# Kernel optimization log

Measured on AMD Instinct MI355X. Metric: run time of the kernel, lower is better.

## Reference

```python
import jax, jax.numpy as jnp
import numpy as np

N = 100000
E = 1000000
IN_C = 128
HID = 128
HEADS = 4
DH = HID // HEADS
L = 2
RWSE_DIM = 16
WALK_LEN = 16
NPAIRS = 200000
EPS = 1e-5


def setup_inputs() -> dict:
    key = jax.random.key(0)
    ks = jax.random.split(key, 20)
    x = jax.random.normal(ks[0], (N, IN_C), dtype=jnp.float32)
    rw_diag = jax.random.uniform(ks[1], (N, WALK_LEN), dtype=jnp.float32)
    edge_index = jax.random.randint(ks[2], (2, E), 0, N, dtype=jnp.int32)
    src = jax.random.randint(ks[3], (NPAIRS,), 0, N, dtype=jnp.int32)
    dst = jax.random.randint(ks[4], (NPAIRS,), 0, N, dtype=jnp.int32)
    s = 0.05
    W_rwse = jax.random.normal(ks[5], (WALK_LEN, RWSE_DIM), dtype=jnp.float32) * s
    b_rwse = jnp.zeros((RWSE_DIM,), dtype=jnp.float32)
    W_in = jax.random.normal(ks[6], (IN_C + RWSE_DIM, HID), dtype=jnp.float32) * s
    b_in = jnp.zeros((HID,), dtype=jnp.float32)
    Wq = jax.random.normal(ks[7], (L, HID, HID), dtype=jnp.float32) * s
    bq = jnp.zeros((L, HID), dtype=jnp.float32)
    Wk = jax.random.normal(ks[8], (L, HID, HID), dtype=jnp.float32) * s
    bk = jnp.zeros((L, HID), dtype=jnp.float32)
    Wv = jax.random.normal(ks[9], (L, HID, HID), dtype=jnp.float32) * s
    bv = jnp.zeros((L, HID), dtype=jnp.float32)
    Ws = jax.random.normal(ks[10], (L, HID, HID), dtype=jnp.float32) * s
    bs = jnp.zeros((L, HID), dtype=jnp.float32)
    ln_g = jnp.ones((L, HID), dtype=jnp.float32)
    ln_b = jnp.zeros((L, HID), dtype=jnp.float32)
    return {"x": x, "rw_diag": rw_diag, "edge_index": edge_index, "src": src,
            "dst": dst, "W_rwse": W_rwse, "b_rwse": b_rwse, "W_in": W_in,
            "b_in": b_in, "Wq": Wq, "bq": bq, "Wk": Wk, "bk": bk, "Wv": Wv,
            "bv": bv, "Ws": Ws, "bs": bs, "ln_g": ln_g, "ln_b": ln_b}


def reference(x, rw_diag, edge_index, src, dst, W_rwse, b_rwse, W_in, b_in,
              Wq, bq, Wk, bk, Wv, bv, Ws, bs, ln_g, ln_b):
    row = edge_index[0]  # message source j
    col = edge_index[1]  # message target i
    # RWSE projection + input projection
    pe = rw_diag @ W_rwse + b_rwse                      # [N, rwse_dim]
    h = jnp.concatenate([x, pe], axis=-1) @ W_in + b_in  # [N, HID]
    scale = 1.0 / jnp.sqrt(jnp.float32(DH))
    for l in range(L):
        q = (h @ Wq[l] + bq[l]).reshape(N, HEADS, DH)
        k = (h @ Wk[l] + bk[l]).reshape(N, HEADS, DH)
        v = (h @ Wv[l] + bv[l]).reshape(N, HEADS, DH)
        # per-edge attention scores (gather)
        score = jnp.einsum('ehd,ehd->eh', q[col], k[row]) * scale  # [E, H]
        # segment softmax over incoming edges of each target node
        m = jax.ops.segment_max(score, col, num_segments=N)   # [N, H]
        ex = jnp.exp(score - m[col])
        z = jax.ops.segment_sum(ex, col, num_segments=N)      # [N, H]
        alpha = ex / z[col]                                   # [E, H]
        agg = jax.ops.segment_sum(alpha[:, :, None] * v[row], col,
                                  num_segments=N).reshape(N, HID)
        conv = agg + h @ Ws[l] + bs[l]  # root/skip linear (PyG lin_skip)
        # residual + LayerNorm + ReLU
        y = h + conv
        mu = jnp.mean(y, axis=-1, keepdims=True)
        var = jnp.mean(jnp.square(y - mu), axis=-1, keepdims=True)
        h = jax.nn.relu(ln_g[l] * (y - mu) / jnp.sqrt(var + EPS) + ln_b[l])
    logits = jnp.sum(h[src] * h[dst], axis=-1)  # [NPAIRS]
    return jax.nn.sigmoid(logits)
```

## Files before the change

### kernel.cpp

```cpp
#include <hip/hip_runtime.h>
#include <hip/hip_bf16.h>
#include <cstdint>


#define NN      100000
#define EE      1000000
#define RWSEC   16
#define WALKC   16
#define NPAIRSC 200000
#define BSH     9
#define BKT     ((NN + 511) >> BSH)

typedef unsigned int       u32;
typedef unsigned short     u16;
typedef unsigned char      u8;
typedef __attribute__((ext_vector_type(8))) short   short8;
typedef __attribute__((ext_vector_type(4))) float   f32x4;

__device__ __forceinline__ float bflo(u32 u){ return __uint_as_float(u << 16); }
__device__ __forceinline__ float bfhi(u32 u){ return __uint_as_float(u & 0xffff0000u); }
__device__ __forceinline__ u16 f2bf(float f){
    u32 u = __float_as_uint(f);
    u += 0x7fffu + ((u >> 16) & 1u);
    return (u16)(u >> 16);
}
__device__ __forceinline__ u32 pack2(float a, float b){
    return (u32)f2bf(a) | ((u32)f2bf(b) << 16);
}

#if defined(__has_builtin)
#if __has_builtin(__builtin_amdgcn_cvt_pk_f32_fp8) && __has_builtin(__builtin_amdgcn_cvt_pk_fp8_f32)
#define HWFP8 1
#endif
#if __has_builtin(__builtin_amdgcn_sdot4)
#define USE_SDOT4 1
#endif
#endif

#ifndef HWFP8
__device__ __forceinline__ float fp8dec1(u32 b){
    u32 s = (b >> 7) & 1u, e = (b >> 3) & 15u, m = b & 7u;
    float mag = e ? __uint_as_float(((e + 120u) << 23) | (m << 20))
                  : (float)m * 0.001953125f;
    return s ? -mag : mag;
}
__device__ __forceinline__ u32 fp8enc1(float f){
    u32 u = __float_as_uint(f); u32 s = (u >> 31) << 7; float a = fabsf(f);
    if (a >= 448.f) return s | 0x7Eu;
    u32 ua = __float_as_uint(a);
    ua += 0x7FFFFu + ((ua >> 20) & 1u);
    int e = (int)(ua >> 23) - 127 + 7;
    if (e <= 0){ int m = (int)rintf(a * 512.f); return s | (u32)m; }
    u32 m = (ua >> 20) & 7u;
    return s | ((u32)e << 3) | m;
}
#endif

__device__ __forceinline__ void fp8x4_dec(u32 w4, float& f0, float& f1, float& f2, float& f3){
#ifdef HWFP8
    auto lo = __builtin_amdgcn_cvt_pk_f32_fp8((int)w4, false);
    auto hi = __builtin_amdgcn_cvt_pk_f32_fp8((int)w4, true);
    f0 = lo[0]; f1 = lo[1]; f2 = hi[0]; f3 = hi[1];
#else
    f0 = fp8dec1(w4 & 255u); f1 = fp8dec1((w4 >> 8) & 255u);
    f2 = fp8dec1((w4 >> 16) & 255u); f3 = fp8dec1(w4 >> 24);
#endif
}
__device__ __forceinline__ u32 fp8x4_enc(float f0, float f1, float f2, float f3){
#ifdef HWFP8
    u32 t = (u32)__builtin_amdgcn_cvt_pk_fp8_f32(f0, f1, 0, false);
    return (u32)__builtin_amdgcn_cvt_pk_fp8_f32(f2, f3, (int)t, true);
#else
    return fp8enc1(f0) | (fp8enc1(f1) << 8) | (fp8enc1(f2) << 16) | (fp8enc1(f3) << 24);
#endif
}

#define QSCALE   48.0f
#define DESCALE  7.67259e-5f

__device__ __forceinline__ int i8q(float f){
    float c = fminf(fmaxf(f * QSCALE, -127.f), 127.f);
    return (int)rintf(c);
}
__device__ __forceinline__ u32 i8x4_enc(float f0, float f1, float f2, float f3){
    return (u32)(i8q(f0) & 255) | ((u32)(i8q(f1) & 255) << 8)
         | ((u32)(i8q(f2) & 255) << 16) | ((u32)(i8q(f3) & 255) << 24);
}

__global__ __launch_bounds__(256) void winprep_kernel(const float* __restrict__ Win,
                                                      u16* __restrict__ Winb){
    int t = blockIdx.x * 256 + threadIdx.x;
    if (t >= 8 * 5 * 64) return;
    int lane = t & 63, fi = t >> 6;
    int nt = fi / 5, kk = fi - nt * 5;
    int col = nt * 16 + (lane & 15);
    int k0  = kk * 32 + (lane >> 4) * 8;
    u16* dst = Winb + (size_t)fi * 512 + lane * 8;
    #pragma unroll
    for (int e = 0; e < 8; ++e){
        int k = k0 + e;
        dst[e] = (k < 144) ? f2bf(Win[(size_t)k * 128 + col]) : (u16)0;
    }
}

__global__ __launch_bounds__(256) void inproj_mfma(const float* __restrict__ x,
        const float* __restrict__ rw, const float* __restrict__ Wr,
        const float* __restrict__ br,
        const u16* __restrict__ Winb, const float* __restrict__ bin,
        u16* __restrict__ hb){
    __shared__ u16   hs[64 * 168];
    __shared__ float rws[64 * 16];
    __shared__ u16   ob[64 * 128];
    int tid = threadIdx.x;
    int n0  = blockIdx.x * 64;

    #pragma unroll
    for (int i = 0; i < 32; ++i){
        int g   = i * 256 + tid;
        int row = g >> 5, c4 = g & 31;
        float4 f = make_float4(0.f, 0.f, 0.f, 0.f);
        if (n0 + row < NN)
            f = *reinterpret_cast<const float4*>(x + (size_t)(n0 + row) * 128 + c4 * 4);
        *reinterpret_cast<uint2*>((char*)hs + row * 336 + c4 * 8)
            = make_uint2(pack2(f.x, f.y), pack2(f.z, f.w));
    }
    {
        int row = tid >> 2, c4 = tid & 3;
        float4 f = make_float4(0.f, 0.f, 0.f, 0.f);
        if (n0 + row < NN)
            f = *reinterpret_cast<const float4*>(rw + (size_t)(n0 + row) * 16 + c4 * 4);
        *reinterpret_cast<float4*>(&rws[row * 16 + c4 * 4]) = f;
    }
    __syncthreads();
    {
        int row = tid >> 2, j0 = (tid & 3) * 4;
        float p0 = br[j0], p1 = br[j0 + 1], p2 = br[j0 + 2], p3 = br[j0 + 3];
        #pragma unroll
        for (int w = 0; w < 16; ++w){
            float r = rws[row * 16 + w];
            const float4 wv = *reinterpret_cast<const float4*>(Wr + w * 16 + j0);
            p0 = fmaf(r, wv.x, p0); p1 = fmaf(r, wv.y, p1);
            p2 = fmaf(r, wv.z, p2); p3 = fmaf(r, wv.w, p3);
        }
        *reinterpret_cast<uint2*>((char*)hs + row * 336 + 256 + (tid & 3) * 8)
            = make_uint2(pack2(p0, p1), pack2(p2, p3));
        *reinterpret_cast<uint2*>((char*)hs + row * 336 + 288 + (tid & 3) * 8)
            = make_uint2(0u, 0u);
    }
    __syncthreads();

    int l = tid & 63, w = tid >> 6;
    int r16 = l & 15, kq = l >> 4;
    short8 ha[4][5];
    #pragma unroll
    for (int rg = 0; rg < 4; ++rg)
        #pragma unroll
        for (int kk = 0; kk < 5; ++kk){
            int row = rg * 16 + r16;
            ha[rg][kk] = *reinterpret_cast<const short8*>(
                (const char*)hs + row * 336 + kk * 64 + kq * 16);
        }
    #pragma unroll
    for (int nt2 = 0; nt2 < 2; ++nt2){
        int nt = w * 2 + nt2;
        const short8* wfrag = reinterpret_cast<const short8*>(Winb) + (size_t)(nt * 5) * 64;
        f32x4 acc[4];
        #pragma unroll
        for (int rg = 0; rg < 4; ++rg) acc[rg] = (f32x4){0.f, 0.f, 0.f, 0.f};
        #pragma unroll
        for (int kk = 0; kk < 5; ++kk){
            short8 wf = wfrag[kk * 64 + l];
            #pragma unroll
            for (int rg = 0; rg < 4; ++rg)
                acc[rg] = __builtin_amdgcn_mfma_f32_16x16x32_bf16(wf, ha[rg][kk], acc[rg], 0, 0, 0);
        }
        float4 bvv = *reinterpret_cast<const float4*>(bin + nt * 16 + kq * 4);
        #pragma unroll
        for (int rg = 0; rg < 4; ++rg){
            u32 p0 = pack2(acc[rg][0] + bvv.x, acc[rg][1] + bvv.y);
            u32 p1 = pack2(acc[rg][2] + bvv.z, acc[rg][3] + bvv.w);
            int row = rg * 16 + r16;
            int cb  = (nt * 32 + kq * 8) ^ ((row & 7) << 4);
            *reinterpret_cast<uint2*>((char*)ob + row * 256 + cb) = make_uint2(p0, p1);
        }
    }
    __syncthreads();
    #pragma unroll
    for (int i = 0; i < 4; ++i){
        int row = i * 16 + (tid >> 4);
        int cb  = (tid & 15) * 16;
        uint4 v = *reinterpret_cast<const uint4*>(
            (char*)ob + row * 256 + (cb ^ ((row & 7) << 4)));
        if (n0 + row < NN)
            *reinterpret_cast<uint4*>(hb + (size_t)(n0 + row) * 128 + cb / 2) = v;
    }
}

__global__ __launch_bounds__(256) void bhist_kernel(const int* __restrict__ col,
                                                    int* __restrict__ bcnt){
    __shared__ int h[BKT];
    int tid = threadIdx.x;
    for (int i = tid; i < BKT; i += 256) h[i] = 0;
    __syncthreads();
    for (int e = blockIdx.x * 256 + tid; e < EE; e += gridDim.x * 256)
        atomicAdd(&h[col[e] >> BSH], 1);
    __syncthreads();
    for (int i = tid; i < BKT; i += 256)
        if (h[i]) atomicAdd(&bcnt[i], h[i]);
}

__global__ __launch_bounds__(256) void bscan_kernel(const int* __restrict__ bcnt,
                                                    int* __restrict__ bstart,
                                                    int* __restrict__ bwork){
    __shared__ int lds[256];
    int tid = threadIdx.x;
    int v = (tid < BKT) ? bcnt[tid] : 0;
    lds[tid] = v;
    __syncthreads();
    for (int off = 1; off < 256; off <<= 1){
        int y = (tid >= off) ? lds[tid - off] : 0;
        __syncthreads();
        lds[tid] += y;
        __syncthreads();
    }
    if (tid < BKT){ int p = lds[tid] - v; bstart[tid] = p; bwork[tid] = p; }
}

__global__ __launch_bounds__(256) void bpart_kernel(const int* __restrict__ ei,
                                                    int* __restrict__ bwork,
                                                    u32* __restrict__ bkt){
    __shared__ int cnt_[BKT], base_[BKT], rnk_[BKT];
    int tid = threadIdx.x;
    for (int i = tid; i < BKT; i += 256){ cnt_[i] = 0; rnk_[i] = 0; }
    __syncthreads();
    for (int e = blockIdx.x * 256 + tid; e < EE; e += gridDim.x * 256)
        atomicAdd(&cnt_[ei[EE + e] >> BSH], 1);
    __syncthreads();
    for (int i = tid; i < BKT; i += 256)
        base_[i] = cnt_[i] ? atomicAdd(&bwork[i], cnt_[i]) : 0;
    __syncthreads();
    for (int e = blockIdx.x * 256 + tid; e < EE; e += gridDim.x * 256){
        int c = ei[EE + e], b = c >> BSH;
        int p = base_[b] + atomicAdd(&rnk_[b], 1);
        bkt[p] = ((u32)ei[e] << BSH) | (u32)(c & 511);
    }
}

__global__ __launch_bounds__(256) void bcsr_kernel(const int* __restrict__ bstart,
                                                   const int* __restrict__ bcnt,
                                                   const u32* __restrict__ bkt,
                                                   int* __restrict__ offs,
                                                   int* __restrict__ deg,
                                                   int* __restrict__ ebuf){
    __shared__ int dcnt[512];
    __shared__ int pref[512];
    __shared__ int psum[256];
    int b   = blockIdx.x;
    int tid = threadIdx.x;
    int n0  = b << BSH;
    int nb  = NN - n0 < 512 ? NN - n0 : 512;
    int e0  = bstart[b];
    int ec  = bcnt[b];
    dcnt[tid] = 0; dcnt[tid + 256] = 0;
    __syncthreads();
    for (int i = tid; i < ec; i += 256)
        atomicAdd(&dcnt[bkt[e0 + i] & 511u], 1);
    __syncthreads();
    int s0 = dcnt[2 * tid], s1 = dcnt[2 * tid + 1];
    psum[tid] = s0 + s1;
    __syncthreads();
    for (int off = 1; off < 256; off <<= 1){
        int y = (tid >= off) ? psum[tid - off] : 0;
        __syncthreads();
        psum[tid] += y;
        __syncthreads();
    }
    int exq = psum[tid] - (s0 + s1);
    pref[2 * tid]     = exq;
    pref[2 * tid + 1] = exq + s0;
    __syncthreads();
    for (int i = tid; i < nb; i += 256){
        offs[n0 + i] = e0 + pref[i];
        deg[n0 + i]  = dcnt[i];
    }
    __syncthreads();
    for (int i = tid; i < ec; i += 256){
        u32 rc = bkt[e0 + i];
        int p = atomicAdd(&pref[rc & 511u], 1);
        ebuf[e0 + p] = (int)(rc >> BSH);
    }
}

__global__ __launch_bounds__(256) void wprep_kernel(const float* __restrict__ Wq,
        const float* __restrict__ Wk, const float* __restrict__ Wv,
        const float* __restrict__ Ws, u16* __restrict__ Wb2){
    int t = blockIdx.x * 256 + threadIdx.x;
    if (t >= 2 * 128 * 64) return;
    int lane = t & 63, fi = (t >> 6) & 127, l = t >> 13;
    int gnt = fi >> 2, kk = fi & 3;
    int m = gnt >> 3;
    int col = (gnt * 16 + (lane & 15)) & 127;
    const float* W = (m == 0 ? Wq : m == 1 ? Wk : m == 2 ? Wv : Ws) + (size_t)l * 16384;
    int k0 = kk * 32 + (lane >> 4) * 8;
    u16* dst = Wb2 + ((size_t)l * 128 + fi) * 512 + lane * 8;
    #pragma unroll
    for (int e = 0; e < 8; ++e) dst[e] = f2bf(W[(size_t)(k0 + e) * 128 + col]);
}

__global__ __launch_bounds__(256) void gemm4_mfma(const u16* __restrict__ hb,
        const u16* __restrict__ Wb2,
        const float* __restrict__ bq, const float* __restrict__ bk,
        const float* __restrict__ bv, const float* __restrict__ bs,
        u16* __restrict__ qb, u8* __restrict__ kvb, u16* __restrict__ hsb){
    __shared__ u16 hs[64 * 128];
    __shared__ u16 ob[4][64 * 128];
    int tid = threadIdx.x;
    int n0  = blockIdx.x * 64;
    #pragma unroll
    for (int i = 0; i < 4; ++i){
        int c = i * 256 + tid;
        int row = c >> 4, cb = (c & 15) * 16;
        uint4 v = make_uint4(0u, 0u, 0u, 0u);
        if (n0 + row < NN)
            v = *reinterpret_cast<const uint4*>(hb + (size_t)(n0 + row) * 128 + cb / 2);
        *reinterpret_cast<uint4*>((char*)hs + row * 256 + (cb ^ ((row & 7) << 4))) = v;
    }
    __syncthreads();
    int l = tid & 63, w = tid >> 6;
    int r16 = l & 15, kq = l >> 4;
    short8 ha[4][4];
    #pragma unroll
    for (int rg = 0; rg < 4; ++rg)
        #pragma unroll
        for (int kk = 0; kk < 4; ++kk){
            int row = rg * 16 + r16;
            int byt = (kk * 64 + kq * 16) ^ ((row & 7) << 4);
            ha[rg][kk] = *reinterpret_cast<const short8*>((const char*)hs + row * 256 + byt);
        }
    const float* bp = w == 0 ? bq : w == 1 ? bk : w == 2 ? bv : bs;
    const short8* wfrag = reinterpret_cast<const short8*>(Wb2) + (size_t)(w * 8) * 4 * 64;
    u16* myob = &ob[w][0];
    #pragma unroll
    for (int nt = 0; nt < 8; ++nt){
        f32x4 acc[4];
        #pragma unroll
        for (int rg = 0; rg < 4; ++rg) acc[rg] = (f32x4){0.f, 0.f, 0.f, 0.f};
        #pragma unroll
        for (int kk = 0; kk < 4; ++kk){
            short8 wf = wfrag[(nt * 4 + kk) * 64 + l];
            #pragma unroll
            for (int rg = 0; rg < 4; ++rg)
                acc[rg] = __builtin_amdgcn_mfma_f32_16x16x32_bf16(wf, ha[rg][kk], acc[rg], 0, 0, 0);
        }
        float4 bvv = *reinterpret_cast<const float4*>(bp + nt * 16 + kq * 4);
        #pragma unroll
        for (int rg = 0; rg < 4; ++rg){
            int row = rg * 16 + r16;
            int cb  = (nt * 32 + kq * 8) ^ ((row & 7) << 4);
            float a0 = acc[rg][0] + bvv.x, a1 = acc[rg][1] + bvv.y;
            float a2 = acc[rg][2] + bvv.z, a3 = acc[rg][3] + bvv.w;
            if (w == 3){
                uint2 hval = *reinterpret_cast<const uint2*>((const char*)hs + row * 256 + cb);
                a0 += bflo(hval.x); a1 += bfhi(hval.x);
                a2 += bflo(hval.y); a3 += bfhi(hval.y);
            }
            *reinterpret_cast<uint2*>((char*)myob + row * 256 + cb)
                = make_uint2(pack2(a0, a1), pack2(a2, a3));
        }
    }
    asm volatile("s_waitcnt lgkmcnt(0)" ::: "memory");
    if (w == 1 || w == 2){
        int off = (w == 2) ? 8 : 0;
        #pragma unroll
        for (int i = 0; i < 16; ++i){
            int row = i * 4 + kq;
            int cb  = r16 * 16;
            uint4 v = *reinterpret_cast<const uint4*>(
                (char*)myob + row * 256 + (cb ^ ((row & 7) << 4)));
            if (n0 + row < NN){
                u32 A, B;
#ifdef USE_SDOT4
                if (w == 1){
                    A = i8x4_enc(bflo(v.x), bfhi(v.x), bflo(v.y), bfhi(v.y));
                    B = i8x4_enc(bflo(v.z), bfhi(v.z), bflo(v.w), bfhi(v.w));
                } else
#endif
                {
                    A = fp8x4_enc(bflo(v.x), bfhi(v.x), bflo(v.y), bfhi(v.y));
                    B = fp8x4_enc(bflo(v.z), bfhi(v.z), bflo(v.w), bfhi(v.w));
                }
                *reinterpret_cast<uint2*>((char*)kvb + (size_t)(n0 + row) * 256
                                          + r16 * 16 + off) = make_uint2(A, B);
            }
        }
    } else {
        u16* outp = (w == 0) ? qb : hsb;
        #pragma unroll
        for (int i = 0; i < 16; ++i){
            int row = i * 4 + kq;
            int cb  = r16 * 16;
            uint4 v = *reinterpret_cast<const uint4*>(
                (char*)myob + row * 256 + (cb ^ ((row & 7) << 4)));
            if (n0 + row < NN)
                *reinterpret_cast<uint4*>(outp + (size_t)(n0 + row) * 128 + cb / 2) = v;
        }
    }
}

__global__ __launch_bounds__(256) void attn_kernel(u16* __restrict__ hb,
        const u16* __restrict__ qb, const u8* __restrict__ kvb,
        const u16* __restrict__ hsb,
        const int* __restrict__ offs, const int* __restrict__ deg,
        const int* __restrict__ ebuf,
        const float* __restrict__ gw, const float* __restrict__ bta){
    int tid  = threadIdx.x;
    int lane = tid & 63;
    int n    = blockIdx.x * 4 + (tid >> 6);
    int eq = lane >> 4, gq = lane & 15;
    uint4 qu = *reinterpret_cast<const uint4*>(qb + (size_t)n * 128 + gq * 8);
#ifdef USE_SDOT4
    int qi0 = (int)i8x4_enc(bflo(qu.x), bfhi(qu.x), bflo(qu.y), bfhi(qu.y));
    int qi1 = (int)i8x4_enc(bflo(qu.z), bfhi(qu.z), bflo(qu.w), bfhi(qu.w));
#else
    const float scale = 0.17677669529663687f;
    float q0 = bflo(qu.x) * scale, q1 = bfhi(qu.x) * scale;
    float q2 = bflo(qu.y) * scale, q3 = bfhi(qu.y) * scale;
    float q4 = bflo(qu.z) * scale, q5 = bfhi(qu.z) * scale;
    float q6 = bflo(qu.w) * scale, q7 = bfhi(qu.w) * scale;
#endif
    int beg = offs[n], cnt = deg[n];
    float z = 0.f;
    float a0 = 0.f, a1 = 0.f, a2 = 0.f, a3 = 0.f;
    float a4 = 0.f, a5 = 0.f, a6 = 0.f, a7 = 0.f;

#ifdef USE_SDOT4
    #define SCORE(kv)                                                                 \
        float s;                                                                      \
        {   int si = __builtin_amdgcn_sdot4((int)kv.x, qi0, 0, false);                \
            si = __builtin_amdgcn_sdot4((int)kv.y, qi1, si, false);                   \
            s = (float)si * DESCALE; }
#else
    #define SCORE(kv)                                                                 \
        float s;                                                                      \
        {   float k0,k1,k2,k3,k4,k5,k6,k7;                                            \
            fp8x4_dec(kv.x, k0, k1, k2, k3); fp8x4_dec(kv.y, k4, k5, k6, k7);         \
            s = q0*k0 + q1*k1 + q2*k2 + q3*k3 + q4*k4 + q5*k5 + q6*k6 + q7*k7; }
#endif

    #define EDGE4(r_)                                                                 \
    {   uint4 kv = *reinterpret_cast<const uint4*>(kvb + (size_t)(r_) * 256 + gq * 16); \
        SCORE(kv);                                                                    \
        s += __shfl_xor(s, 1); s += __shfl_xor(s, 2);                                 \
        float ex = __expf(s);                                                         \
        float v0,v1,v2,v3,v4,v5,v6,v7;                                                \
        fp8x4_dec(kv.z, v0, v1, v2, v3); fp8x4_dec(kv.w, v4, v5, v6, v7);             \
        z += ex;                                                                      \
        a0 = fmaf(ex, v0, a0); a1 = fmaf(ex, v1, a1);                                 \
        a2 = fmaf(ex, v2, a2); a3 = fmaf(ex, v3, a3);                                 \
        a4 = fmaf(ex, v4, a4); a5 = fmaf(ex, v5, a5);                                 \
        a6 = fmaf(ex, v6, a6); a7 = fmaf(ex, v7, a7);  }

    int t = 0;
    for (; t + 8 <= cnt; t += 8){
        int ra = ebuf[beg + t + eq];
        int rb = ebuf[beg + t + 4 + eq];
        EDGE4(ra);
        EDGE4(rb);
    }
    if (t + 4 <= cnt){
        int ra = ebuf[beg + t + eq];
        EDGE4(ra);
        t += 4;
    }
    if (t < cnt){
        int idx = t + eq;
        int r = ebuf[beg + (idx < cnt ? idx : cnt - 1)];
        uint4 kv = *reinterpret_cast<const uint4*>(kvb + (size_t)r * 256 + gq * 16);
        SCORE(kv);
        s += __shfl_xor(s, 1); s += __shfl_xor(s, 2);
        float ex = (idx < cnt) ? __expf(s) : 0.f;
        float v0,v1,v2,v3,v4,v5,v6,v7;
        fp8x4_dec(kv.z, v0, v1, v2, v3); fp8x4_dec(kv.w, v4, v5, v6, v7);
        z += ex;
        a0 = fmaf(ex, v0, a0); a1 = fmaf(ex, v1, a1);
        a2 = fmaf(ex, v2, a2); a3 = fmaf(ex, v3, a3);
        a4 = fmaf(ex, v4, a4); a5 = fmaf(ex, v5, a5);
        a6 = fmaf(ex, v6, a6); a7 = fmaf(ex, v7, a7);
    }
    #undef EDGE4
    #undef SCORE

    z  += __shfl_xor(z, 16);  z  += __shfl_xor(z, 32);
    a0 += __shfl_xor(a0, 16); a0 += __shfl_xor(a0, 32);
    a1 += __shfl_xor(a1, 16); a1 += __shfl_xor(a1, 32);
    a2 += __shfl_xor(a2, 16); a2 += __shfl_xor(a2, 32);
    a3 += __shfl_xor(a3, 16); a3 += __shfl_xor(a3, 32);
    a4 += __shfl_xor(a4, 16); a4 += __shfl_xor(a4, 32);
    a5 += __shfl_xor(a5, 16); a5 += __shfl_xor(a5, 32);
    a6 += __shfl_xor(a6, 16); a6 += __shfl_xor(a6, 32);
    a7 += __shfl_xor(a7, 16); a7 += __shfl_xor(a7, 32);
    float rz = (cnt > 0) ? 1.f / z : 0.f;

    size_t p = (size_t)n * 128 + gq * 8;
    uint4 hu = *reinterpret_cast<const uint4*>(hsb + p);
    float y0 = bflo(hu.x) + a0 * rz, y1 = bfhi(hu.x) + a1 * rz;
    float y2 = bflo(hu.y) + a2 * rz, y3 = bfhi(hu.y) + a3 * rz;
    float y4 = bflo(hu.z) + a4 * rz, y5 = bfhi(hu.z) + a5 * rz;
    float y6 = bflo(hu.w) + a6 * rz, y7 = bfhi(hu.w) + a7 * rz;
    float sum = y0 + y1 + y2 + y3 + y4 + y5 + y6 + y7;
    float sq  = y0*y0 + y1*y1 + y2*y2 + y3*y3 + y4*y4 + y5*y5 + y6*y6 + y7*y7;
    #pragma unroll
    for (int m = 1; m < 16; m <<= 1){
        sum += __shfl_xor(sum, m);
        sq  += __shfl_xor(sq,  m);
    }
    float mu  = sum * (1.f / 128.f);
    float var = sq * (1.f / 128.f) - mu * mu;
    var = var < 0.f ? 0.f : var;
    float inv = rsqrtf(var + 1e-5f);
    int c = gq * 8;
    float4 gm0 = *reinterpret_cast<const float4*>(gw + c);
    float4 gm1 = *reinterpret_cast<const float4*>(gw + c + 4);
    float4 bt0 = *reinterpret_cast<const float4*>(bta + c);
    float4 bt1 = *reinterpret_cast<const float4*>(bta + c + 4);
    float o0 = fmaf(gm0.x * (y0 - mu), inv, bt0.x);
    float o1 = fmaf(gm0.y * (y1 - mu), inv, bt0.y);
    float o2 = fmaf(gm0.z * (y2 - mu), inv, bt0.z);
    float o3 = fmaf(gm0.w * (y3 - mu), inv, bt0.w);
    float o4 = fmaf(gm1.x * (y4 - mu), inv, bt1.x);
    float o5 = fmaf(gm1.y * (y5 - mu), inv, bt1.y);
    float o6 = fmaf(gm1.z * (y6 - mu), inv, bt1.z);
    float o7 = fmaf(gm1.w * (y7 - mu), inv, bt1.w);
    o0 = o0 > 0.f ? o0 : 0.f;  o1 = o1 > 0.f ? o1 : 0.f;
    o2 = o2 > 0.f ? o2 : 0.f;  o3 = o3 > 0.f ? o3 : 0.f;
    o4 = o4 > 0.f ? o4 : 0.f;  o5 = o5 > 0.f ? o5 : 0.f;
    o6 = o6 > 0.f ? o6 : 0.f;  o7 = o7 > 0.f ? o7 : 0.f;
    if (eq == 0)
        *reinterpret_cast<uint4*>(hb + p) = make_uint4(
            pack2(o0, o1), pack2(o2, o3), pack2(o4, o5), pack2(o6, o7));
}

__global__ __launch_bounds__(256) void pair_kernel(const u16* __restrict__ hb,
                                                   const int* __restrict__ src,
                                                   const int* __restrict__ dst,
                                                   float* __restrict__ out){
    int tid = threadIdx.x;
    int pid = blockIdx.x * 16 + (tid >> 4);
    int sub = tid & 15;
    int s = src[pid], d = dst[pid];
    uint4 a = *reinterpret_cast<const uint4*>(hb + (size_t)s * 128 + sub * 8);
    uint4 b = *reinterpret_cast<const uint4*>(hb + (size_t)d * 128 + sub * 8);
    float dot = bflo(a.x) * bflo(b.x) + bfhi(a.x) * bfhi(b.x)
              + bflo(a.y) * bflo(b.y) + bfhi(a.y) * bfhi(b.y)
              + bflo(a.z) * bflo(b.z) + bfhi(a.z) * bfhi(b.z)
              + bflo(a.w) * bflo(b.w) + bfhi(a.w) * bfhi(b.w);
    dot += __shfl_xor(dot, 1); dot += __shfl_xor(dot, 2);
    dot += __shfl_xor(dot, 4); dot += __shfl_xor(dot, 8);
    if (sub == 0) out[pid] = 1.f / (1.f + __expf(-dot));
}

extern "C" void kernel_launch(void* const* d_in, const int* in_sizes, int n_in,
                              void* d_out, int out_size, void* d_ws, size_t ws_size,
                              hipStream_t stream){
    const float* x      = (const float*)d_in[0];
    const float* rw     = (const float*)d_in[1];
    const int*   ei     = (const int*)  d_in[2];
    const int*   src    = (const int*)  d_in[3];
    const int*   dst    = (const int*)  d_in[4];
    const float* W_rwse = (const float*)d_in[5];
    const float* b_rwse = (const float*)d_in[6];
    const float* W_in   = (const float*)d_in[7];
    const float* b_in   = (const float*)d_in[8];
    const float* Wq     = (const float*)d_in[9];
    const float* bq     = (const float*)d_in[10];
    const float* Wk     = (const float*)d_in[11];
    const float* bk     = (const float*)d_in[12];
    const float* Wv     = (const float*)d_in[13];
    const float* bv     = (const float*)d_in[14];
    const float* Wsk    = (const float*)d_in[15];
    const float* bsk    = (const float*)d_in[16];
    const float* ln_g   = (const float*)d_in[17];
    const float* ln_b   = (const float*)d_in[18];
    float* out = (float*)d_out;

    char* p = (char*)d_ws;
    auto carve = [&](size_t bytes) -> char* {
        char* r = p; p += (bytes + 255) & ~(size_t)255; return r;
    };
    u16*   hb    = (u16*) carve((size_t)NN * 128 * 2);
    u16*   qb    = (u16*) carve((size_t)NN * 128 * 2);
    u8*    kvb   = (u8*)  carve((size_t)NN * 256);
    u16*   hsb   = (u16*) carve((size_t)NN * 128 * 2);
    int*   offs  = (int*) carve((size_t)NN * 4);
    int*   deg   = (int*) carve((size_t)NN * 4);
    int*   ebuf  = (int*) carve((size_t)EE * 4);
    u32*   bkt   = (u32*) carve((size_t)EE * 4);
    int*   bcnt  = (int*) carve((size_t)BKT * 4);
    int*   bstart= (int*) carve((size_t)BKT * 4);
    int*   bwork = (int*) carve((size_t)BKT * 4);
    u16*   Wb2   = (u16*) carve((size_t)2 * 128 * 512 * 2);
    u16*   Winb  = (u16*) carve((size_t)8 * 5 * 512 * 2);

    hipMemsetAsync(bcnt, 0, (size_t)BKT * 4, stream);

    winprep_kernel<<<10, 256, 0, stream>>>(W_in, Winb);
    wprep_kernel<<<64, 256, 0, stream>>>(Wq, Wk, Wv, Wsk, Wb2);
    inproj_mfma<<<(NN + 63) / 64, 256, 0, stream>>>(x, rw, W_rwse, b_rwse,
                                                    Winb, b_in, hb);
    bhist_kernel<<<512, 256, 0, stream>>>(ei + EE, bcnt);
    bscan_kernel<<<1, 256, 0, stream>>>(bcnt, bstart, bwork);
    bpart_kernel<<<512, 256, 0, stream>>>(ei, bwork, bkt);
    bcsr_kernel<<<BKT, 256, 0, stream>>>(bstart, bcnt, bkt, offs, deg, ebuf);

    for (int l = 0; l < 2; ++l){
        gemm4_mfma<<<(NN + 63) / 64, 256, 0, stream>>>(hb, Wb2 + (size_t)l * 65536,
            bq + l * 128, bk + l * 128, bv + l * 128, bsk + l * 128,
            qb, kvb, hsb);
        attn_kernel<<<NN / 4, 256, 0, stream>>>(hb, qb, kvb, hsb,
            offs, deg, ebuf, ln_g + l * 128, ln_b + l * 128);
    }
    pair_kernel<<<NPAIRSC / 16, 256, 0, stream>>>(hb, src, dst, out);
}
```

Measured before the change: 340.9 us.

## Store Q as int8, accumulate attention values in packed fp16

The GEMM kernel now quantizes Q to int8 at write time, so the attention kernel reads 8 bytes per lane instead of 16 and skips re-quantizing. The attention accumulation switches from eight fp32 FMAs per edge to four packed fp16 FMAs, with fp8 values converted straight to half pairs. Softmax uses exp2 with the log2(e) factor folded into the descale constant, and the tail edge path reuses the same macro. The fp16 accumulators and unnormalized exp weights risk precision loss or overflow on high-degree nodes.

After: 334.2 us. About the same (-2.0%).

```diff
diff --git a/kernel.cpp b/kernel.cpp
--- a/kernel.cpp
+++ b/kernel.cpp
@@ -14,8 +14,9 @@
 typedef unsigned int       u32;
 typedef unsigned short     u16;
 typedef unsigned char      u8;
-typedef __attribute__((ext_vector_type(8))) short   short8;
-typedef __attribute__((ext_vector_type(4))) float   f32x4;
+typedef __attribute__((ext_vector_type(8))) short    short8;
+typedef __attribute__((ext_vector_type(4))) float    f32x4;
+typedef __attribute__((ext_vector_type(2))) _Float16 h2;
 
 __device__ __forceinline__ float bflo(u32 u){ return __uint_as_float(u << 16); }
 __device__ __forceinline__ float bfhi(u32 u){ return __uint_as_float(u & 0xffff0000u); }
@@ -34,6 +35,9 @@
 #endif
 #if __has_builtin(__builtin_amdgcn_sdot4)
 #define USE_SDOT4 1
+#endif
+#if __has_builtin(__builtin_amdgcn_cvt_pk_f16_fp8)
+#define HWF16FP8 1
 #endif
 #endif
 
@@ -74,9 +78,25 @@
     return fp8enc1(f0) | (fp8enc1(f1) << 8) | (fp8enc1(f2) << 16) | (fp8enc1(f3) << 24);
 #endif
 }
-
-#define QSCALE   48.0f
-#define DESCALE  7.67259e-5f
+__device__ __forceinline__ void fp8x4_to_h2(u32 w, h2& lo, h2& hi){
+#ifdef HWF16FP8
+    lo = __builtin_bit_cast(h2, __builtin_amdgcn_cvt_pk_f16_fp8((int)w, false));
+    hi = __builtin_bit_cast(h2, __builtin_amdgcn_cvt_pk_f16_fp8((int)w, true));
+#else
+    float f0, f1, f2, f3;
+    fp8x4_dec(w, f0, f1, f2, f3);
+    lo = __builtin_bit_cast(h2, __builtin_amdgcn_cvt_pkrtz(f0, f1));
+    hi = __builtin_bit_cast(h2, __builtin_amdgcn_cvt_pkrtz(f2, f3));
+#endif
+}
+__device__ __forceinline__ h2 h2shfl_add(h2 a, int m){
+    int u = __builtin_bit_cast(int, a);
+    int o = __shfl_xor(u, m);
+    return a + __builtin_bit_cast(h2, o);
+}
+
+#define QSCALE    48.0f
+#define DESCALE2  1.10693e-4f
 
 __device__ __forceinline__ int i8q(float f){
     float c = fminf(fmaxf(f * QSCALE, -127.f), 127.f);
@@ -85,6 +105,9 @@
 __device__ __forceinline__ u32 i8x4_enc(float f0, float f1, float f2, float f3){
     return (u32)(i8q(f0) & 255) | ((u32)(i8q(f1) & 255) << 8)
          | ((u32)(i8q(f2) & 255) << 16) | ((u32)(i8q(f3) & 255) << 24);
+}
+__device__ __forceinline__ float sb(u32 w, int i){
+    return (float)(int)(signed char)((w >> (i * 8)) & 255u);
 }
 
 __global__ __launch_bounds__(256) void winprep_kernel(const float* __restrict__ Win,
@@ -311,7 +334,7 @@
         const u16* __restrict__ Wb2,
         const float* __restrict__ bq, const float* __restrict__ bk,
         const float* __restrict__ bv, const float* __restrict__ bs,
-        u16* __restrict__ qb, u8* __restrict__ kvb, u16* __restrict__ hsb){
+        u8* __restrict__ qb, u8* __restrict__ kvb, u16* __restrict__ hsb){
     __shared__ u16 hs[64 * 128];
     __shared__ u16 ob[4][64 * 128];
     int tid = threadIdx.x;
@@ -393,8 +416,25 @@
                                           + r16 * 16 + off) = make_uint2(A, B);
             }
         }
+    } else if (w == 0){
+        #pragma unroll
+        for (int i = 0; i < 16; ++i){
+            int row = i * 4 + kq;
+            int cb  = r16 * 16;
+            uint4 v = *reinterpret_cast<const uint4*>(
+                (char*)myob + row * 256 + (cb ^ ((row & 7) << 4)));
+            if (n0 + row < NN){
+#ifdef USE_SDOT4
+                u32 A = i8x4_enc(bflo(v.x), bfhi(v.x), bflo(v.y), bfhi(v.y));
+                u32 B = i8x4_enc(bflo(v.z), bfhi(v.z), bflo(v.w), bfhi(v.w));
+                *reinterpret_cast<uint2*>(qb + (size_t)(n0 + row) * 128 + cb / 2)
+                    = make_uint2(A, B);
+#else
+                *reinterpret_cast<uint4*>((u16*)qb + (size_t)(n0 + row) * 128 + cb / 2) = v;
+#endif
+            }
+        }
     } else {
-        u16* outp = (w == 0) ? qb : hsb;
         #pragma unroll
         for (int i = 0; i < 16; ++i){
             int row = i * 4 + kq;
@@ -402,13 +442,13 @@
             uint4 v = *reinterpret_cast<const uint4*>(
                 (char*)myob + row * 256 + (cb ^ ((row & 7) << 4)));
             if (n0 + row < NN)
-                *reinterpret_cast<uint4*>(outp + (size_t)(n0 + row) * 128 + cb / 2) = v;
+                *reinterpret_cast<uint4*>(hsb + (size_t)(n0 + row) * 128 + cb / 2) = v;
         }
     }
 }
 
 __global__ __launch_bounds__(256) void attn_kernel(u16* __restrict__ hb,
-        const u16* __restrict__ qb, const u8* __restrict__ kvb,
+        const u8* __restrict__ qb, const u8* __restrict__ kvb,
         const u16* __restrict__ hsb,
         const int* __restrict__ offs, const int* __restrict__ deg,
         const int* __restrict__ ebuf,
@@ -417,12 +457,12 @@
     int lane = tid & 63;
     int n    = blockIdx.x * 4 + (tid >> 6);
     int eq = lane >> 4, gq = lane & 15;
-    uint4 qu = *reinterpret_cast<const uint4*>(qb + (size_t)n * 128 + gq * 8);
 #ifdef USE_SDOT4
-    int qi0 = (int)i8x4_enc(bflo(qu.x), bfhi(qu.x), bflo(qu.y), bfhi(qu.y));
-    int qi1 = (int)i8x4_enc(bflo(qu.z), bfhi(qu.z), bflo(qu.w), bfhi(qu.w));
+    uint2 qu = *reinterpret_cast<const uint2*>(qb + (size_t)n * 128 + gq * 8);
+    int qi0 = (int)qu.x, qi1 = (int)qu.y;
 #else
     const float scale = 0.17677669529663687f;
+    uint4 qu = *reinterpret_cast<const uint4*>((const u16*)qb + (size_t)n * 128 + gq * 8);
     float q0 = bflo(qu.x) * scale, q1 = bfhi(qu.x) * scale;
     float q2 = bflo(qu.y) * scale, q3 = bfhi(qu.y) * scale;
     float q4 = bflo(qu.z) * scale, q5 = bfhi(qu.z) * scale;
@@ -430,76 +470,68 @@
 #endif
     int beg = offs[n], cnt = deg[n];
     float z = 0.f;
-    float a0 = 0.f, a1 = 0.f, a2 = 0.f, a3 = 0.f;
-    float a4 = 0.f, a5 = 0.f, a6 = 0.f, a7 = 0.f;
+    h2 acc01 = (h2)0, acc23 = (h2)0, acc45 = (h2)0, acc67 = (h2)0;
 
 #ifdef USE_SDOT4
     #define SCORE(kv)                                                                 \
         float s;                                                                      \
         {   int si = __builtin_amdgcn_sdot4((int)kv.x, qi0, 0, false);                \
             si = __builtin_amdgcn_sdot4((int)kv.y, qi1, si, false);                   \
-            s = (float)si * DESCALE; }
+            s = (float)si * DESCALE2; }
 #else
     #define SCORE(kv)                                                                 \
         float s;                                                                      \
-        {   float k0,k1,k2,k3,k4,k5,k6,k7;                                            \
-            fp8x4_dec(kv.x, k0, k1, k2, k3); fp8x4_dec(kv.y, k4, k5, k6, k7);         \
-            s = q0*k0 + q1*k1 + q2*k2 + q3*k3 + q4*k4 + q5*k5 + q6*k6 + q7*k7; }
-#endif
-
-    #define EDGE4(r_)                                                                 \
+        {   s = q0*sb(kv.x,0) + q1*sb(kv.x,1) + q2*sb(kv.x,2) + q3*sb(kv.x,3)         \
+              + q4*sb(kv.y,0) + q5*sb(kv.y,1) + q6*sb(kv.y,2) + q7*sb(kv.y,3);        \
+            s *= (1.4426950408889634f / QSCALE); }
+#endif
+
+    #define EDGE4(r_, ok_)                                                            \
     {   uint4 kv = *reinterpret_cast<const uint4*>(kvb + (size_t)(r_) * 256 + gq * 16); \
         SCORE(kv);                                                                    \
         s += __shfl_xor(s, 1); s += __shfl_xor(s, 2);                                 \
-        float ex = __expf(s);                                                         \
-        float v0,v1,v2,v3,v4,v5,v6,v7;                                                \
-        fp8x4_dec(kv.z, v0, v1, v2, v3); fp8x4_dec(kv.w, v4, v5, v6, v7);             \
+        float ex = (ok_) ? exp2f(s) : 0.f;                                            \
+        h2 v01, v23, v45, v67;                                                        \
+        fp8x4_to_h2(kv.z, v01, v23);                                                  \
+        fp8x4_to_h2(kv.w, v45, v67);                                                  \
         z += ex;                                                                      \
-        a0 = fmaf(ex, v0, a0); a1 = fmaf(ex, v1, a1);                                 \
-        a2 = fmaf(ex, v2, a2); a3 = fmaf(ex, v3, a3);                                 \
-        a4 = fmaf(ex, v4, a4); a5 = fmaf(ex, v5, a5);                                 \
-        a6 = fmaf(ex, v6, a6); a7 = fmaf(ex, v7, a7);  }
+        _Float16 exh = (_Float16)ex;                                                  \
+        h2 exv = {exh, exh};                                                          \
+        acc01 = __builtin_elementwise_fma(exv, v01, acc01);                           \
+        acc23 = __builtin_elementwise_fma(exv, v23, acc23);                           \
+        acc45 = __builtin_elementwise_fma(exv, v45, acc45);                           \
+        acc67 = __builtin_elementwise_fma(exv, v67, acc67);  }
 
     int t = 0;
     for (; t + 8 <= cnt; t += 8){
         int ra = ebuf[beg + t + eq];
         int rb = ebuf[beg + t + 4 + eq];
-        EDGE4(ra);
-        EDGE4(rb);
+        EDGE4(ra, true);
+        EDGE4(rb, true);
     }
     if (t + 4 <= cnt){
         int ra = ebuf[beg + t + eq];
-        EDGE4(ra);
+        EDGE4(ra, true);
         t += 4;
     }
     if (t < cnt){
         int idx = t + eq;
         int r = ebuf[beg + (idx < cnt ? idx : cnt - 1)];
-        uint4 kv = *reinterpret_cast<const uint4*>(kvb + (size_t)r * 256 + gq * 16);
-        SCORE(kv);
-        s += __shfl_xor(s, 1); s += __shfl_xor(s, 2);
-        float ex = (idx < cnt) ? __expf(s) : 0.f;
-        float v0,v1,v2,v3,v4,v5,v6,v7;
-        fp8x4_dec(kv.z, v0, v1, v2, v3); fp8x4_dec(kv.w, v4, v5, v6, v7);
-        z += ex;
-        a0 = fmaf(ex, v0, a0); a1 = fmaf(ex, v1, a1);
-        a2 = fmaf(ex, v2, a2); a3 = fmaf(ex, v3, a3);
-        a4 = fmaf(ex, v4, a4); a5 = fmaf(ex, v5, a5);
-        a6 = fmaf(ex, v6, a6); a7 = fmaf(ex, v7, a7);
+        EDGE4(r, idx < cnt);
     }
     #undef EDGE4
     #undef SCORE
 
-    z  += __shfl_xor(z, 16);  z  += __shfl_xor(z, 32);
-    a0 += __shfl_xor(a0, 16); a0 += __shfl_xor(a0, 32);
-    a1 += __shfl_xor(a1, 16); a1 += __shfl_xor(a1, 32);
-    a2 += __shfl_xor(a2, 16); a2 += __shfl_xor(a2, 32);
-    a3 += __shfl_xor(a3, 16); a3 += __shfl_xor(a3, 32);
-    a4 += __shfl_xor(a4, 16); a4 += __shfl_xor(a4, 32);
-    a5 += __shfl_xor(a5, 16); a5 += __shfl_xor(a5, 32);
-    a6 += __shfl_xor(a6, 16); a6 += __shfl_xor(a6, 32);
-    a7 += __shfl_xor(a7, 16); a7 += __shfl_xor(a7, 32);
+    z += __shfl_xor(z, 16);  z += __shfl_xor(z, 32);
+    acc01 = h2shfl_add(acc01, 16); acc01 = h2shfl_add(acc01, 32);
+    acc23 = h2shfl_add(acc23, 16); acc23 = h2shfl_add(acc23, 32);
+    acc45 = h2shfl_add(acc45, 16); acc45 = h2shfl_add(acc45, 32);
+    acc67 = h2shfl_add(acc67, 16); acc67 = h2shfl_add(acc67, 32);
     float rz = (cnt > 0) ? 1.f / z : 0.f;
+    float a0 = (float)acc01[0], a1 = (float)acc01[1];
+    float a2 = (float)acc23[0], a3 = (float)acc23[1];
+    float a4 = (float)acc45[0], a5 = (float)acc45[1];
+    float a6 = (float)acc67[0], a7 = (float)acc67[1];
 
     size_t p = (size_t)n * 128 + gq * 8;
     uint4 hu = *reinterpret_cast<const uint4*>(hsb + p);
@@ -588,7 +620,7 @@
         char* r = p; p += (bytes + 255) & ~(size_t)255; return r;
     };
     u16*   hb    = (u16*) carve((size_t)NN * 128 * 2);
-    u16*   qb    = (u16*) carve((size_t)NN * 128 * 2);
+    u8*    qb    = (u8*)  carve((size_t)NN * 128 * 2);
     u8*    kvb   = (u8*)  carve((size_t)NN * 256);
     u16*   hsb   = (u16*) carve((size_t)NN * 128 * 2);
     int*   offs  = (int*) carve((size_t)NN * 4);
```
